# Performance work log

Hardware: AMD Instinct MI355X
Metric: run time of the kernel (lower is better)

The kernel has to match this reference:

```python
import jax, jax.numpy as jnp
import numpy as np


def setup_inputs() -> dict:
    key = jax.random.key(0)
    k1, = jax.random.split(key, 1)
    inputs = jax.random.normal(k1, (16, 64, 64, 512), dtype=jnp.float32)
    gamma = jnp.zeros((1,), dtype=jnp.float32)
    return {"inputs": inputs, "gamma": gamma}


def reference(inputs, gamma):
    # inputs: [B, H, W, C] (NHWC)
    B, H, W, C = inputs.shape
    vec_a = inputs.reshape(B, H * W, C)              # [B, N, C], N = H*W
    # channel Gram matrix: aTa[b, i, j] = sum_n a[b, n, i] * a[b, n, j]
    aTa = jnp.einsum('bni,bnj->bij', vec_a, vec_a)    # [B, C, C]
    attn = jax.nn.softmax(aTa, axis=-1)               # softmax over last axis
    # aaTa = attn @ vec_a^T -> [B, C, N]; transpose -> [B, N, C]
    aaTa = jnp.einsum('bij,bnj->bni', attn, vec_a)    # [B, N, C]
    aaTa = aaTa.reshape(B, H, W, C)
    return gamma * aaTa + inputs
```

## Files before the change

kernel.cpp:

```cpp
#include <hip/hip_runtime.h>

#define BATCH 16
#define NPIX  4096
#define CCH   512
#define NSPLIT 8
#define KSPL  (NPIX / NSPLIT)
#define NUT   10

using bf16x8   = __attribute__((ext_vector_type(8))) __bf16;
using floatx4  = __attribute__((ext_vector_type(4))) float;
using ushort8v = __attribute__((ext_vector_type(8))) unsigned short;
using ushort4v = __attribute__((ext_vector_type(4))) unsigned short;

static __device__ __forceinline__ unsigned short f2bf(float f) {
    unsigned u = __builtin_bit_cast(unsigned, f);
    unsigned r = 0x7fffu + ((u >> 16) & 1u);
    return (unsigned short)((u + r) >> 16);
}
static __device__ __forceinline__ float bf2f(unsigned short v) {
    unsigned u = ((unsigned)v) << 16;
    return __builtin_bit_cast(float, u);
}
static __device__ __forceinline__ bf16x8 ld_frag(const unsigned short* p) {
    return __builtin_bit_cast(bf16x8, *(const ushort8v*)p);
}
static __device__ __forceinline__ void gld16(const unsigned short* g, unsigned short* l) {
    __builtin_amdgcn_global_load_lds(
        (const __attribute__((address_space(1))) void*)g,
        (__attribute__((address_space(3))) void*)l,
        16, 0, 0);
}

__global__ __launch_bounds__(256) void k_cvt(const float* __restrict__ inp,
                                             unsigned short* __restrict__ Abf,
                                             unsigned short* __restrict__ AT) {
    __shared__ unsigned short sN[64 * 66];
    const int bn = blockIdx.x, bc = blockIdx.y, b = blockIdx.z;
    const int t  = threadIdx.x;
    const int n0 = bn * 64, c0 = bc * 64;
    const float* ip = inp + ((size_t)b * NPIX + n0) * CCH + c0;
    unsigned short* op = Abf + ((size_t)b * NPIX + n0) * CCH + c0;

#pragma unroll
    for (int r = 0; r < 2; ++r) {
        int n  = r * 32 + (t >> 3);
        int c8 = (t & 7) * 8;
        float4 v0 = *(const float4*)(ip + (size_t)n * CCH + c8);
        float4 v1 = *(const float4*)(ip + (size_t)n * CCH + c8 + 4);
        ushort8v w;
        w[0] = f2bf(v0.x); w[1] = f2bf(v0.y); w[2] = f2bf(v0.z); w[3] = f2bf(v0.w);
        w[4] = f2bf(v1.x); w[5] = f2bf(v1.y); w[6] = f2bf(v1.z); w[7] = f2bf(v1.w);
        *(ushort8v*)(op + (size_t)n * CCH + c8) = w;
        *(ushort8v*)&sN[n * 66 + c8] = w;
    }
    __syncthreads();

    const int cp = t >> 3;
    const int ng = (t & 7) * 8;
    ushort8v o0, o1;
#pragma unroll
    for (int k = 0; k < 8; ++k) {
        unsigned d = *(const unsigned*)&sN[(ng + k) * 66 + cp * 2];
        o0[k] = (unsigned short)(d & 0xffffu);
        o1[k] = (unsigned short)(d >> 16);
    }
    unsigned short* tp = AT + ((size_t)b * CCH + c0) * NPIX + n0;
    *(ushort8v*)(tp + (size_t)(cp * 2)     * NPIX + ng) = o0;
    *(ushort8v*)(tp + (size_t)(cp * 2 + 1) * NPIX + ng) = o1;
}

__global__ __launch_bounds__(256) void k_ata(const unsigned short* __restrict__ AT,
                                             unsigned short* __restrict__ Sp) {
    __shared__ unsigned short sA[128 * 32];
    __shared__ unsigned short sB[128 * 32];
    const int u = blockIdx.x, s = blockIdx.y, b = blockIdx.z;
    const int ti = (u < 4) ? 0 : (u < 7) ? 1 : (u < 9) ? 2 : 3;
    const int u0 = ti * 5 - (ti * (ti + 1)) / 2;
    const int tj = ti + (u - u0);
    const unsigned short* pa = AT + ((size_t)b * CCH + ti * 128) * NPIX + s * KSPL;
    const unsigned short* pb = AT + ((size_t)b * CCH + tj * 128) * NPIX + s * KSPL;
    const int tid = threadIdx.x, lane = tid & 63, wave = tid >> 6;
    const int lrow = lane >> 2;
    const int lk   = (lane & 3) * 8;

    floatx4 acc[2][8];
#pragma unroll
    for (int tm = 0; tm < 2; ++tm)
#pragma unroll
        for (int tn = 0; tn < 8; ++tn)
            acc[tm][tn] = floatx4{0.f, 0.f, 0.f, 0.f};

    for (int k0 = 0; k0 < KSPL; k0 += 32) {
#pragma unroll
        for (int i = 0; i < 2; ++i) {
            const int r = wave * 32 + i * 16;
            gld16(pa + (size_t)(r + lrow) * NPIX + k0 + lk, &sA[r * 32]);
            gld16(pb + (size_t)(r + lrow) * NPIX + k0 + lk, &sB[r * 32]);
        }
        __syncthreads();

        const int kq = (lane >> 4) * 8;
        bf16x8 af[2], bv[8];
#pragma unroll
        for (int tm = 0; tm < 2; ++tm)
            af[tm] = ld_frag(&sA[(wave * 32 + tm * 16 + (lane & 15)) * 32 + kq]);
#pragma unroll
        for (int tn = 0; tn < 8; ++tn)
            bv[tn] = ld_frag(&sB[(tn * 16 + (lane & 15)) * 32 + kq]);
#pragma unroll
        for (int tm = 0; tm < 2; ++tm)
#pragma unroll
            for (int tn = 0; tn < 8; ++tn)
                acc[tm][tn] = __builtin_amdgcn_mfma_f32_16x16x32_bf16(
                    af[tm], bv[tn], acc[tm][tn], 0, 0, 0);
        __syncthreads();
    }

    unsigned short* Tb = Sp + ((((size_t)s * BATCH + b) * NUT + u) << 14);
#pragma unroll
    for (int tm = 0; tm < 2; ++tm)
#pragma unroll
        for (int tn = 0; tn < 8; ++tn) {
            ushort4v w;
#pragma unroll
            for (int r = 0; r < 4; ++r) w[r] = f2bf(acc[tm][tn][r]);
            *(ushort4v*)&Tb[((((wave * 2 + tm) * 8 + tn) * 64) + lane) * 4] = w;
        }
}

__global__ __launch_bounds__(256) void k_softmax(const unsigned short* __restrict__ Sp,
                                                 unsigned short* __restrict__ P) {
    __shared__ float red[6];
    const int row = blockIdx.x;
    const int b = row >> 9, i = row & 511;
    const int tid = threadIdx.x, lane = tid & 63, wave = tid >> 6;
    const size_t sstr = (size_t)BATCH * NUT * 16384;

    float x[2];
#pragma unroll
    for (int e = 0; e < 2; ++e) {
        const int j  = tid + e * 256;
        const int ti = i >> 7, tj = j >> 7;
        const int il = i & 127, jl = j & 127;
        const bool sw = ti > tj;
        const int a  = sw ? tj : ti;
        const int cm = sw ? ti : tj;
        const int u  = a * 4 + cm - ((a * (a + 1)) >> 1);
        const int rr = sw ? jl : il;
        const int cc = sw ? il : jl;
        const int off = ((((rr >> 4) * 8 + (cc >> 4)) * 64) +
                         ((rr >> 2) & 3) * 16 + (cc & 15)) * 4 + (rr & 3);
        const size_t base = (((size_t)b * NUT + u) << 14) + off;
        float v = 0.f;
#pragma unroll
        for (int s = 0; s < NSPLIT; ++s) v += bf2f(Sp[base + s * sstr]);
        x[e] = v;
    }

    float m = fmaxf(x[0], x[1]);
#pragma unroll
    for (int o = 32; o; o >>= 1) m = fmaxf(m, __shfl_xor(m, o, 64));
    if (lane == 0) red[wave] = m;
    __syncthreads();
    if (tid == 0) red[4] = fmaxf(fmaxf(red[0], red[1]), fmaxf(red[2], red[3]));
    __syncthreads();
    m = red[4];

    float e0 = __expf(x[0] - m), e1 = __expf(x[1] - m);
    float sum = e0 + e1;
#pragma unroll
    for (int o = 32; o; o >>= 1) sum += __shfl_xor(sum, o, 64);
    if (lane == 0) red[wave] = sum;
    __syncthreads();
    if (tid == 0) red[5] = red[0] + red[1] + red[2] + red[3];
    __syncthreads();
    float inv = 1.0f / red[5];

    P[(size_t)row * CCH + tid]       = f2bf(e0 * inv);
    P[(size_t)row * CCH + tid + 256] = f2bf(e1 * inv);
}

__global__ __launch_bounds__(256) void k_av(const unsigned short* __restrict__ Abf,
                                            const unsigned short* __restrict__ P,
                                            const float* __restrict__ inp,
                                            const float* __restrict__ gamma,
                                            float* __restrict__ out) {
    __shared__ unsigned short sA[128 * 32];
    __shared__ unsigned short sB[128 * 32];
    const int bn = blockIdx.x, bi = blockIdx.y, b = blockIdx.z;
    const unsigned short* pa = Abf + ((size_t)b * NPIX + bn * 128) * CCH;
    const unsigned short* pb = P + ((size_t)b * CCH + bi * 128) * CCH;
    const int tid = threadIdx.x, lane = tid & 63, wave = tid >> 6;
    const int lrow = lane >> 2;
    const int lk   = (lane & 3) * 8;
    const float g = gamma[0];

    floatx4 acc[2][8];
#pragma unroll
    for (int tm = 0; tm < 2; ++tm)
#pragma unroll
        for (int tn = 0; tn < 8; ++tn)
            acc[tm][tn] = floatx4{0.f, 0.f, 0.f, 0.f};

    for (int k0 = 0; k0 < CCH; k0 += 32) {
#pragma unroll
        for (int i = 0; i < 2; ++i) {
            const int r = wave * 32 + i * 16;
            gld16(pa + (size_t)(r + lrow) * CCH + k0 + lk, &sA[r * 32]);
            gld16(pb + (size_t)(r + lrow) * CCH + k0 + lk, &sB[r * 32]);
        }
        __syncthreads();

        const int kq = (lane >> 4) * 8;
        bf16x8 af[2], bv[8];
#pragma unroll
        for (int tm = 0; tm < 2; ++tm)
            af[tm] = ld_frag(&sA[(wave * 32 + tm * 16 + (lane & 15)) * 32 + kq]);
#pragma unroll
        for (int tn = 0; tn < 8; ++tn)
            bv[tn] = ld_frag(&sB[(tn * 16 + (lane & 15)) * 32 + kq]);
#pragma unroll
        for (int tm = 0; tm < 2; ++tm)
#pragma unroll
            for (int tn = 0; tn < 8; ++tn)
                acc[tm][tn] = __builtin_amdgcn_mfma_f32_16x16x32_bf16(
                    af[tm], bv[tn], acc[tm][tn], 0, 0, 0);
        __syncthreads();
    }

    float* Ob = out + ((size_t)b * NPIX + bn * 128) * CCH + bi * 128;
    const float* Ib = inp + ((size_t)b * NPIX + bn * 128) * CCH + bi * 128;
#pragma unroll
    for (int tm = 0; tm < 2; ++tm)
#pragma unroll
        for (int tn = 0; tn < 8; ++tn)
#pragma unroll
            for (int r = 0; r < 4; ++r) {
                int nrow = wave * 32 + tm * 16 + (lane >> 4) * 4 + r;
                int icol = tn * 16 + (lane & 15);
                size_t o = (size_t)nrow * CCH + icol;
                Ob[o] = g * acc[tm][tn][r] + Ib[o];
            }
}

extern "C" void kernel_launch(void* const* d_in, const int* in_sizes, int n_in,
                              void* d_out, int out_size, void* d_ws, size_t ws_size,
                              hipStream_t stream) {
    const float* inp   = (const float*)d_in[0];
    const float* gamma = (const float*)d_in[1];
    float* out = (float*)d_out;

    char* ws = (char*)d_ws;
    unsigned short* Abf = (unsigned short*)ws;
    unsigned short* AT  = (unsigned short*)(ws + (size_t)67108864);
    unsigned short* Sp  = (unsigned short*)(ws + (size_t)134217728);
    unsigned short* P   = (unsigned short*)(ws + (size_t)134217728 + 41943040);

    k_cvt<<<dim3(NPIX / 64, CCH / 64, BATCH), 256, 0, stream>>>(inp, Abf, AT);
    k_ata<<<dim3(NUT, NSPLIT, BATCH), 256, 0, stream>>>(AT, Sp);
    k_softmax<<<BATCH * CCH, 256, 0, stream>>>(Sp, P);
    k_av<<<dim3(NPIX / 128, CCH / 128, BATCH), 256, 0, stream>>>(Abf, P, inp, gamma, out);
}
```

Before: 413.2 us.

## Double-buffer LDS tiles and swizzle block order in Gram and AV GEMMs

Both GEMM kernels now use two LDS buffers, so the global-to-LDS load of the next K tile is issued before the MFMAs on the current tile, and one barrier per iteration is dropped. The intent is to overlap memory latency with compute. Block indices are also remapped with a stride-8 swizzle so that neighbouring workgroups touch different batches or tiles, which may spread work more evenly across XCDs and L2 caches. LDS use per block doubles, which can lower occupancy.

```diff
diff --git a/kernel.cpp b/kernel.cpp
--- a/kernel.cpp
+++ b/kernel.cpp
@@ -71,9 +71,14 @@
 
 __global__ __launch_bounds__(256) void k_ata(const unsigned short* __restrict__ AT,
                                              unsigned short* __restrict__ Sp) {
-    __shared__ unsigned short sA[128 * 32];
-    __shared__ unsigned short sB[128 * 32];
-    const int u = blockIdx.x, s = blockIdx.y, b = blockIdx.z;
+    __shared__ unsigned short sA[2][128 * 32];
+    __shared__ unsigned short sB[2][128 * 32];
+    const int orig = blockIdx.x + gridDim.x * (blockIdx.y + gridDim.y * blockIdx.z);
+    const int swz  = (orig & 7) * (NUT * NSPLIT * BATCH / 8) + (orig >> 3);
+    const int u = swz % NUT;
+    const int s = (swz / NUT) % NSPLIT;
+    const int b = swz / (NUT * NSPLIT);
+
     const int ti = (u < 4) ? 0 : (u < 7) ? 1 : (u < 9) ? 2 : 3;
     const int u0 = ti * 5 - (ti * (ti + 1)) / 2;
     const int tj = ti + (u - u0);
@@ -90,23 +95,33 @@
         for (int tn = 0; tn < 8; ++tn)
             acc[tm][tn] = floatx4{0.f, 0.f, 0.f, 0.f};
 
-    for (int k0 = 0; k0 < KSPL; k0 += 32) {
-#pragma unroll
-        for (int i = 0; i < 2; ++i) {
-            const int r = wave * 32 + i * 16;
-            gld16(pa + (size_t)(r + lrow) * NPIX + k0 + lk, &sA[r * 32]);
-            gld16(pb + (size_t)(r + lrow) * NPIX + k0 + lk, &sB[r * 32]);
+#pragma unroll
+    for (int i = 0; i < 2; ++i) {
+        const int r = wave * 32 + i * 16;
+        gld16(pa + (size_t)(r + lrow) * NPIX + lk, &sA[0][r * 32]);
+        gld16(pb + (size_t)(r + lrow) * NPIX + lk, &sB[0][r * 32]);
+    }
+    __syncthreads();
+
+    int cur = 0;
+    for (int t = 0; t < KSPL / 32; ++t) {
+        if (t < KSPL / 32 - 1) {
+            const int k0 = (t + 1) * 32;
+#pragma unroll
+            for (int i = 0; i < 2; ++i) {
+                const int r = wave * 32 + i * 16;
+                gld16(pa + (size_t)(r + lrow) * NPIX + k0 + lk, &sA[cur ^ 1][r * 32]);
+                gld16(pb + (size_t)(r + lrow) * NPIX + k0 + lk, &sB[cur ^ 1][r * 32]);
+            }
         }
-        __syncthreads();
-
         const int kq = (lane >> 4) * 8;
         bf16x8 af[2], bv[8];
 #pragma unroll
         for (int tm = 0; tm < 2; ++tm)
-            af[tm] = ld_frag(&sA[(wave * 32 + tm * 16 + (lane & 15)) * 32 + kq]);
-#pragma unroll
-        for (int tn = 0; tn < 8; ++tn)
-            bv[tn] = ld_frag(&sB[(tn * 16 + (lane & 15)) * 32 + kq]);
+            af[tm] = ld_frag(&sA[cur][(wave * 32 + tm * 16 + (lane & 15)) * 32 + kq]);
+#pragma unroll
+        for (int tn = 0; tn < 8; ++tn)
+            bv[tn] = ld_frag(&sB[cur][(tn * 16 + (lane & 15)) * 32 + kq]);
 #pragma unroll
         for (int tm = 0; tm < 2; ++tm)
 #pragma unroll
@@ -114,6 +129,7 @@
                 acc[tm][tn] = __builtin_amdgcn_mfma_f32_16x16x32_bf16(
                     af[tm], bv[tn], acc[tm][tn], 0, 0, 0);
         __syncthreads();
+        cur ^= 1;
     }
 
     unsigned short* Tb = Sp + ((((size_t)s * BATCH + b) * NUT + u) << 14);
@@ -185,9 +201,14 @@
                                             const float* __restrict__ inp,
                                             const float* __restrict__ gamma,
                                             float* __restrict__ out) {
-    __shared__ unsigned short sA[128 * 32];
-    __shared__ unsigned short sB[128 * 32];
-    const int bn = blockIdx.x, bi = blockIdx.y, b = blockIdx.z;
+    __shared__ unsigned short sA[2][128 * 32];
+    __shared__ unsigned short sB[2][128 * 32];
+    const int orig = blockIdx.x + gridDim.x * (blockIdx.y + gridDim.y * blockIdx.z);
+    const int swz  = (orig & 7) * ((NPIX / 128) * (CCH / 128) * BATCH / 8) + (orig >> 3);
+    const int bn = swz % (NPIX / 128);
+    const int bi = (swz / (NPIX / 128)) % (CCH / 128);
+    const int b  = swz / ((NPIX / 128) * (CCH / 128));
+
     const unsigned short* pa = Abf + ((size_t)b * NPIX + bn * 128) * CCH;
     const unsigned short* pb = P + ((size_t)b * CCH + bi * 128) * CCH;
     const int tid = threadIdx.x, lane = tid & 63, wave = tid >> 6;
@@ -202,23 +223,33 @@
         for (int tn = 0; tn < 8; ++tn)
             acc[tm][tn] = floatx4{0.f, 0.f, 0.f, 0.f};
 
-    for (int k0 = 0; k0 < CCH; k0 += 32) {
-#pragma unroll
-        for (int i = 0; i < 2; ++i) {
-            const int r = wave * 32 + i * 16;
-            gld16(pa + (size_t)(r + lrow) * CCH + k0 + lk, &sA[r * 32]);
-            gld16(pb + (size_t)(r + lrow) * CCH + k0 + lk, &sB[r * 32]);
+#pragma unroll
+    for (int i = 0; i < 2; ++i) {
+        const int r = wave * 32 + i * 16;
+        gld16(pa + (size_t)(r + lrow) * CCH + lk, &sA[0][r * 32]);
+        gld16(pb + (size_t)(r + lrow) * CCH + lk, &sB[0][r * 32]);
+    }
+    __syncthreads();
+
+    int cur = 0;
+    for (int t = 0; t < CCH / 32; ++t) {
+        if (t < CCH / 32 - 1) {
+            const int k0 = (t + 1) * 32;
+#pragma unroll
+            for (int i = 0; i < 2; ++i) {
+                const int r = wave * 32 + i * 16;
+                gld16(pa + (size_t)(r + lrow) * CCH + k0 + lk, &sA[cur ^ 1][r * 32]);
+                gld16(pb + (size_t)(r + lrow) * CCH + k0 + lk, &sB[cur ^ 1][r * 32]);
+            }
         }
-        __syncthreads();
-
         const int kq = (lane >> 4) * 8;
         bf16x8 af[2], bv[8];
 #pragma unroll
         for (int tm = 0; tm < 2; ++tm)
-            af[tm] = ld_frag(&sA[(wave * 32 + tm * 16 + (lane & 15)) * 32 + kq]);
-#pragma unroll
-        for (int tn = 0; tn < 8; ++tn)
-            bv[tn] = ld_frag(&sB[(tn * 16 + (lane & 15)) * 32 + kq]);
+            af[tm] = ld_frag(&sA[cur][(wave * 32 + tm * 16 + (lane & 15)) * 32 + kq]);
+#pragma unroll
+        for (int tn = 0; tn < 8; ++tn)
+            bv[tn] = ld_frag(&sB[cur][(tn * 16 + (lane & 15)) * 32 + kq]);
 #pragma unroll
         for (int tm = 0; tm < 2; ++tm)
 #pragma unroll
@@ -226,6 +257,7 @@
                 acc[tm][tn] = __builtin_amdgcn_mfma_f32_16x16x32_bf16(
                     af[tm], bv[tn], acc[tm][tn], 0, 0, 0);
         __syncthreads();
+        cur ^= 1;
     }
 
     float* Ob = out + ((size_t)b * NPIX + bn * 128) * CCH + bi * 128;
```

Result: slower. 460.8 us (+11.5%).

## Double-buffer LDS tiles and swizzle block order in Gram and AV GEMMs

Applied to the files above, without the earlier changes.

Both GEMM kernels (k_ata and k_av) now use two LDS buffers per operand, so the async global-to-LDS loads for the next K-slice are issued before computing on the current slice, and one barrier per stage is removed. Block indices are also remapped with an 8-way swizzle that spreads consecutive workgroups across XCDs/batches. This aims to hide global load latency behind MFMA work. In exchange, LDS use per block doubles, which may lower occupancy.

```diff
diff --git a/kernel.cpp b/kernel.cpp
--- a/kernel.cpp
+++ b/kernel.cpp
@@ -71,9 +71,16 @@
 
 __global__ __launch_bounds__(256) void k_ata(const unsigned short* __restrict__ AT,
                                              unsigned short* __restrict__ Sp) {
-    __shared__ unsigned short sA[128 * 32];
-    __shared__ unsigned short sB[128 * 32];
-    const int u = blockIdx.x, s = blockIdx.y, b = blockIdx.z;
+    __shared__ unsigned short sA0[128 * 32];
+    __shared__ unsigned short sA1[128 * 32];
+    __shared__ unsigned short sB0[128 * 32];
+    __shared__ unsigned short sB1[128 * 32];
+    const int orig = blockIdx.x + gridDim.x * (blockIdx.y + gridDim.y * blockIdx.z);
+    const int swz  = (orig & 7) * (NUT * NSPLIT * BATCH / 8) + (orig >> 3);
+    const int u = swz % NUT;
+    const int s = (swz / NUT) % NSPLIT;
+    const int b = swz / (NUT * NSPLIT);
+
     const int ti = (u < 4) ? 0 : (u < 7) ? 1 : (u < 9) ? 2 : 3;
     const int u0 = ti * 5 - (ti * (ti + 1)) / 2;
     const int tj = ti + (u - u0);
@@ -90,31 +97,47 @@
         for (int tn = 0; tn < 8; ++tn)
             acc[tm][tn] = floatx4{0.f, 0.f, 0.f, 0.f};
 
-    for (int k0 = 0; k0 < KSPL; k0 += 32) {
-#pragma unroll
-        for (int i = 0; i < 2; ++i) {
-            const int r = wave * 32 + i * 16;
-            gld16(pa + (size_t)(r + lrow) * NPIX + k0 + lk, &sA[r * 32]);
-            gld16(pb + (size_t)(r + lrow) * NPIX + k0 + lk, &sB[r * 32]);
-        }
+#define ATA_STAGE(DA, DB, K0)                                                  \
+    {                                                                          \
+        _Pragma("unroll")                                                      \
+        for (int i = 0; i < 2; ++i) {                                          \
+            const int r = wave * 32 + i * 16;                                  \
+            gld16(pa + (size_t)(r + lrow) * NPIX + (K0) + lk, &DA[r * 32]);    \
+            gld16(pb + (size_t)(r + lrow) * NPIX + (K0) + lk, &DB[r * 32]);    \
+        }                                                                      \
+    }
+
+#define ATA_COMP(SA, SB)                                                       \
+    {                                                                          \
+        const int kq = (lane >> 4) * 8;                                        \
+        bf16x8 af[2], bv[8];                                                   \
+        _Pragma("unroll")                                                      \
+        for (int tm = 0; tm < 2; ++tm)                                         \
+            af[tm] = ld_frag(&SA[(wave * 32 + tm * 16 + (lane & 15)) * 32 + kq]); \
+        _Pragma("unroll")                                                      \
+        for (int tn = 0; tn < 8; ++tn)                                         \
+            bv[tn] = ld_frag(&SB[(tn * 16 + (lane & 15)) * 32 + kq]);          \
+        _Pragma("unroll")                                                      \
+        for (int tm = 0; tm < 2; ++tm)                                         \
+            _Pragma("unroll")                                                  \
+            for (int tn = 0; tn < 8; ++tn)                                     \
+                acc[tm][tn] = __builtin_amdgcn_mfma_f32_16x16x32_bf16(         \
+                    af[tm], bv[tn], acc[tm][tn], 0, 0, 0);                     \
+    }
+
+    ATA_STAGE(sA0, sB0, 0)
+    __syncthreads();
+
+    for (int t = 0; t < KSPL / 32; t += 2) {
+        ATA_STAGE(sA1, sB1, (t + 1) * 32)
+        ATA_COMP(sA0, sB0)
         __syncthreads();
-
-        const int kq = (lane >> 4) * 8;
-        bf16x8 af[2], bv[8];
-#pragma unroll
-        for (int tm = 0; tm < 2; ++tm)
-            af[tm] = ld_frag(&sA[(wave * 32 + tm * 16 + (lane & 15)) * 32 + kq]);
-#pragma unroll
-        for (int tn = 0; tn < 8; ++tn)
-            bv[tn] = ld_frag(&sB[(tn * 16 + (lane & 15)) * 32 + kq]);
-#pragma unroll
-        for (int tm = 0; tm < 2; ++tm)
-#pragma unroll
-            for (int tn = 0; tn < 8; ++tn)
-                acc[tm][tn] = __builtin_amdgcn_mfma_f32_16x16x32_bf16(
-                    af[tm], bv[tn], acc[tm][tn], 0, 0, 0);
+        if (t + 2 < KSPL / 32) ATA_STAGE(sA0, sB0, (t + 2) * 32)
+        ATA_COMP(sA1, sB1)
         __syncthreads();
     }
+#undef ATA_STAGE
+#undef ATA_COMP
 
     unsigned short* Tb = Sp + ((((size_t)s * BATCH + b) * NUT + u) << 14);
 #pragma unroll
@@ -185,9 +208,16 @@
                                             const float* __restrict__ inp,
                                             const float* __restrict__ gamma,
                                             float* __restrict__ out) {
-    __shared__ unsigned short sA[128 * 32];
-    __shared__ unsigned short sB[128 * 32];
-    const int bn = blockIdx.x, bi = blockIdx.y, b = blockIdx.z;
+    __shared__ unsigned short sA0[128 * 32];
+    __shared__ unsigned short sA1[128 * 32];
+    __shared__ unsigned short sB0[128 * 32];
+    __shared__ unsigned short sB1[128 * 32];
+    const int orig = blockIdx.x + gridDim.x * (blockIdx.y + gridDim.y * blockIdx.z);
+    const int swz  = (orig & 7) * ((NPIX / 128) * (CCH / 128) * BATCH / 8) + (orig >> 3);
+    const int bn = swz % (NPIX / 128);
+    const int bi = (swz / (NPIX / 128)) % (CCH / 128);
+    const int b  = swz / ((NPIX / 128) * (CCH / 128));
+
     const unsigned short* pa = Abf + ((size_t)b * NPIX + bn * 128) * CCH;
     const unsigned short* pb = P + ((size_t)b * CCH + bi * 128) * CCH;
     const int tid = threadIdx.x, lane = tid & 63, wave = tid >> 6;
@@ -202,31 +232,47 @@
         for (int tn = 0; tn < 8; ++tn)
             acc[tm][tn] = floatx4{0.f, 0.f, 0.f, 0.f};
 
-    for (int k0 = 0; k0 < CCH; k0 += 32) {
-#pragma unroll
-        for (int i = 0; i < 2; ++i) {
-            const int r = wave * 32 + i * 16;
-            gld16(pa + (size_t)(r + lrow) * CCH + k0 + lk, &sA[r * 32]);
-            gld16(pb + (size_t)(r + lrow) * CCH + k0 + lk, &sB[r * 32]);
-        }
+#define AV_STAGE(DA, DB, K0)                                                   \
+    {                                                                          \
+        _Pragma("unroll")                                                      \
+        for (int i = 0; i < 2; ++i) {                                          \
+            const int r = wave * 32 + i * 16;                                  \
+            gld16(pa + (size_t)(r + lrow) * CCH + (K0) + lk, &DA[r * 32]);     \
+            gld16(pb + (size_t)(r + lrow) * CCH + (K0) + lk, &DB[r * 32]);     \
+        }                                                                      \
+    }
+
+#define AV_COMP(SA, SB)                                                        \
+    {                                                                          \
+        const int kq = (lane >> 4) * 8;                                        \
+        bf16x8 af[2], bv[8];                                                   \
+        _Pragma("unroll")                                                      \
+        for (int tm = 0; tm < 2; ++tm)                                         \
+            af[tm] = ld_frag(&SA[(wave * 32 + tm * 16 + (lane & 15)) * 32 + kq]); \
+        _Pragma("unroll")                                                      \
+        for (int tn = 0; tn < 8; ++tn)                                         \
+            bv[tn] = ld_frag(&SB[(tn * 16 + (lane & 15)) * 32 + kq]);          \
+        _Pragma("unroll")                                                      \
+        for (int tm = 0; tm < 2; ++tm)                                         \
+            _Pragma("unroll")                                                  \
+            for (int tn = 0; tn < 8; ++tn)                                     \
+                acc[tm][tn] = __builtin_amdgcn_mfma_f32_16x16x32_bf16(         \
+                    af[tm], bv[tn], acc[tm][tn], 0, 0, 0);                     \
+    }
+
+    AV_STAGE(sA0, sB0, 0)
+    __syncthreads();
+
+    for (int t = 0; t < CCH / 32; t += 2) {
+        AV_STAGE(sA1, sB1, (t + 1) * 32)
+        AV_COMP(sA0, sB0)
         __syncthreads();
-
-        const int kq = (lane >> 4) * 8;
-        bf16x8 af[2], bv[8];
-#pragma unroll
-        for (int tm = 0; tm < 2; ++tm)
-            af[tm] = ld_frag(&sA[(wave * 32 + tm * 16 + (lane & 15)) * 32 + kq]);
-#pragma unroll
-        for (int tn = 0; tn < 8; ++tn)
-            bv[tn] = ld_frag(&sB[(tn * 16 + (lane & 15)) * 32 + kq]);
-#pragma unroll
-        for (int tm = 0; tm < 2; ++tm)
-#pragma unroll
-            for (int tn = 0; tn < 8; ++tn)
-                acc[tm][tn] = __builtin_amdgcn_mfma_f32_16x16x32_bf16(
-                    af[tm], bv[tn], acc[tm][tn], 0, 0, 0);
+        if (t + 2 < CCH / 32) AV_STAGE(sA0, sB0, (t + 2) * 32)
+        AV_COMP(sA1, sB1)
         __syncthreads();
     }
+#undef AV_STAGE
+#undef AV_COMP
 
     float* Ob = out + ((size_t)b * NPIX + bn * 128) * CCH + bi * 128;
     const float* Ib = inp + ((size_t)b * NPIX + bn * 128) * CCH + bi * 128;
```

Measured after the change: 461.6 us. 11.7% more time.
